# Kernel optimization log

Hardware: AMD Instinct MI355X
Metric: run time of the kernel (lower is better)

Reference implementation:

```python
import jax, jax.numpy as jnp
import numpy as np

B, S, D = 8, 1024, 1024
NEG = -1e9


def setup_inputs() -> dict:
    key = jax.random.key(0)
    ks = jax.random.split(key, 6)
    context = jax.random.normal(ks[0], (B, S, D), dtype=jnp.float32)
    eos_mask = jax.random.randint(ks[1], (B, S, S), 0, 2).astype(jnp.int32)
    scale = 1.0 / np.sqrt(D).astype(np.float32)
    Wq = jax.random.normal(ks[2], (D, D), dtype=jnp.float32) * scale
    bq = jnp.zeros((D,), jnp.float32)
    Wk = jax.random.normal(ks[3], (D, D), dtype=jnp.float32) * scale
    bk = jnp.zeros((D,), jnp.float32)
    ln_a = jnp.ones((D,), jnp.float32)
    ln_b = jnp.zeros((D,), jnp.float32)
    return dict(context=context, eos_mask=eos_mask, Wq=Wq, bq=bq, Wk=Wk, bk=bk,
                ln_a=ln_a, ln_b=ln_b)


def _forward(context, eos_mask, Wq, bq, Wk, bk, ln_a, ln_b):
    d_model = context.shape[-1]
    seq_len = context.shape[1]
    # LayerNorm with torch-style unbiased std (ddof=1)
    mean = context.mean(-1, keepdims=True)
    var = ((context - mean) ** 2).sum(-1, keepdims=True) / (d_model - 1)
    x = ln_a * (context - mean) / (jnp.sqrt(var) + 1e-6) + ln_b

    a = jnp.eye(seq_len, k=1, dtype=jnp.int32)    # super-diagonal
    b = jnp.eye(seq_len, k=0, dtype=jnp.int32)    # diagonal
    c = jnp.eye(seq_len, k=-1, dtype=jnp.int32)   # sub-diagonal
    tri = jnp.triu(jnp.ones((seq_len, seq_len), jnp.float32), 0)

    mask = eos_mask & (a + c)  # [B,S,S] banded + eos mask

    q = x @ Wq.T + bq
    k = x @ Wk.T + bk
    scores = jnp.einsum('bsd,btd->bst', q, k) / d_model
    scores = jnp.where(mask == 0, NEG, scores)
    neibor = jax.nn.softmax(scores, axis=-1)
    neibor = jnp.sqrt(neibor * jnp.swapaxes(neibor, -2, -1) + 1e-9)

    # log-space triangular matmul 'scan'
    t = jnp.where(a == 0, 0.0, jnp.log(neibor + 1e-9)) @ tri  # [B,S,S]
    g = jnp.exp(jnp.einsum('st,btu->bsu', tri, t))
    strict_upper = tri.astype(jnp.int32) - b
    g = jnp.where(strict_upper == 0, 0.0, g)
    g = g + jnp.swapaxes(g, -2, -1) + jnp.where(b == 0, 1e-9, neibor)
    return g, neibor


def reference(context, eos_mask, Wq, bq, Wk, bk, ln_a, ln_b):
    return _forward(context, eos_mask, Wq, bq, Wk, bk, ln_a, ln_b)
```

## Files before the change

kernel.cpp:

```cpp
#include <hip/hip_runtime.h>
#include <math.h>

#define B_ 8
#define S_ 1024
#define D_ 1024
constexpr int BS = B_ * S_;

typedef short bf16x8 __attribute__((ext_vector_type(8)));
typedef float f32x4 __attribute__((ext_vector_type(4)));

__device__ __forceinline__ unsigned short f2bf(float f) {
    unsigned int u = __float_as_uint(f);
    u += 0x7fffu + ((u >> 16) & 1u);
    return (unsigned short)(u >> 16);
}
__device__ __forceinline__ float bf2f(unsigned short h) {
    return __uint_as_float(((unsigned int)h) << 16);
}

__device__ __forceinline__ float block_reduce_sum(float val, float* sh) {
    int tid = threadIdx.x;
    int lane = tid & 63, w = tid >> 6;
    #pragma unroll
    for (int off = 32; off > 0; off >>= 1) val += __shfl_down(val, off, 64);
    if (lane == 0) sh[w] = val;
    __syncthreads();
    int nw = blockDim.x >> 6;
    float total = 0.f;
    for (int i = 0; i < nw; i++) total += sh[i];
    __syncthreads();
    return total;
}

__global__ void ln_kernel(const float* __restrict__ ctx,
                          const float* __restrict__ ln_a,
                          const float* __restrict__ ln_b,
                          unsigned short* __restrict__ xb) {
    __shared__ float sh[4];
    int r = blockIdx.x;
    int tid = threadIdx.x;
    const float* row = ctx + (size_t)r * D_;
    float v[4];
    float s = 0.f;
    #pragma unroll
    for (int i = 0; i < 4; i++) { v[i] = row[tid + i * 256]; s += v[i]; }
    float total = block_reduce_sum(s, sh);
    float mean = total * (1.0f / D_);
    float sq = 0.f;
    #pragma unroll
    for (int i = 0; i < 4; i++) { float d = v[i] - mean; sq += d * d; }
    float varsum = block_reduce_sum(sq, sh);
    float var = varsum * (1.0f / (D_ - 1));
    float inv = 1.0f / (sqrtf(var) + 1e-6f);
    unsigned short* orow = xb + (size_t)r * D_;
    #pragma unroll
    for (int i = 0; i < 4; i++) {
        int d = tid + i * 256;
        orow[d] = f2bf(ln_a[d] * (v[i] - mean) * inv + ln_b[d]);
    }
}

__global__ void transpose2_bf16(const float* __restrict__ inq,
                                const float* __restrict__ ink,
                                unsigned short* __restrict__ outq,
                                unsigned short* __restrict__ outk) {
    __shared__ float t[32][33];
    const float* in = blockIdx.z ? ink : inq;
    unsigned short* out = blockIdx.z ? outk : outq;
    int bx = blockIdx.x * 32, by = blockIdx.y * 32;
    int tx = threadIdx.x, ty = threadIdx.y;
    #pragma unroll
    for (int i = 0; i < 32; i += 8)
        t[ty + i][tx] = in[(size_t)(by + ty + i) * D_ + bx + tx];
    __syncthreads();
    #pragma unroll
    for (int i = 0; i < 32; i += 8)
        out[(size_t)(bx + ty + i) * D_ + by + tx] = f2bf(t[tx][ty + i]);
}

__global__ void bias_terms(const float* __restrict__ Wq, const float* __restrict__ Wk,
                           const float* __restrict__ bq, const float* __restrict__ bk,
                           float* __restrict__ u, float* __restrict__ v,
                           float* __restrict__ c0) {
    int b = blockIdx.x;
    int tid = threadIdx.x;
    float ua[4] = {}, va[4] = {};
    int d0 = b * 128;
    for (int d = d0; d < d0 + 128; d++) {
        float bqd = bq[d], bkd = bk[d];
        const float* wkr = Wk + (size_t)d * D_;
        const float* wqr = Wq + (size_t)d * D_;
        #pragma unroll
        for (int i = 0; i < 4; i++) {
            int c = tid + i * 256;
            ua[i] += wkr[c] * bqd;
            va[i] += wqr[c] * bkd;
        }
    }
    #pragma unroll
    for (int i = 0; i < 4; i++) {
        atomicAdd(&u[tid + i * 256], ua[i]);
        atomicAdd(&v[tid + i * 256], va[i]);
    }
    if (tid < 128) atomicAdd(c0, bq[d0 + tid] * bk[d0 + tid]);
}

__global__ __launch_bounds__(256) void gemm_bt64(
    const unsigned short* __restrict__ A,
    const unsigned short* __restrict__ Bt,
    unsigned short* __restrict__ C,
    int M, int N, int K) {
    __shared__ __align__(16) unsigned short As[64 * 64];
    __shared__ __align__(16) unsigned short Bs[64 * 64];
    const int tid = threadIdx.x;
    const int wave = tid >> 6, lane = tid & 63;
    const int bm = blockIdx.y * 64, bn = blockIdx.x * 64;
    const int lrow8 = lane >> 3;
    const int pchunk = lane & 7;
    const int m_lane = lane & 15, quad = lane >> 4;
    const int wr = wave >> 1, wc = wave & 1;

    f32x4 acc[2][2] = {};

    for (int k0 = 0; k0 < K; k0 += 64) {
        #pragma unroll
        for (int c = 0; c < 2; c++) {
            int row = wave * 16 + c * 8 + lrow8;
            int gchunk = pchunk ^ (row & 7);
            const unsigned short* gpA = A + (size_t)(bm + row) * K + k0 + gchunk * 8;
            const unsigned short* gpB = Bt + (size_t)(bn + row) * K + k0 + gchunk * 8;
            __builtin_amdgcn_global_load_lds(
                (const __attribute__((address_space(1))) void*)gpA,
                (__attribute__((address_space(3))) void*)(As + (wave * 16 + c * 8) * 64),
                16, 0, 0);
            __builtin_amdgcn_global_load_lds(
                (const __attribute__((address_space(1))) void*)gpB,
                (__attribute__((address_space(3))) void*)(Bs + (wave * 16 + c * 8) * 64),
                16, 0, 0);
        }
        __syncthreads();
        #pragma unroll
        for (int kk = 0; kk < 2; kk++) {
            bf16x8 af[2], bfr[2];
            #pragma unroll
            for (int i = 0; i < 2; i++) {
                int row = wr * 32 + i * 16 + m_lane;
                int lchunk = kk * 4 + quad;
                af[i] = *(const bf16x8*)(As + row * 64 + (lchunk ^ (row & 7)) * 8);
            }
            #pragma unroll
            for (int j = 0; j < 2; j++) {
                int row = wc * 32 + j * 16 + m_lane;
                int lchunk = kk * 4 + quad;
                bfr[j] = *(const bf16x8*)(Bs + row * 64 + (lchunk ^ (row & 7)) * 8);
            }
            #pragma unroll
            for (int i = 0; i < 2; i++)
                #pragma unroll
                for (int j = 0; j < 2; j++)
                    acc[i][j] = __builtin_amdgcn_mfma_f32_16x16x32_bf16(
                        af[i], bfr[j], acc[i][j], 0, 0, 0);
        }
        __syncthreads();
    }
    #pragma unroll
    for (int i = 0; i < 2; i++)
        #pragma unroll
        for (int j = 0; j < 2; j++)
            #pragma unroll
            for (int r = 0; r < 4; r++) {
                int row = bm + wr * 32 + i * 16 + quad * 4 + r;
                int col = bn + wc * 32 + j * 16 + m_lane;
                C[(size_t)row * N + col] = f2bf(acc[i][j][r]);
            }
}

__global__ __launch_bounds__(256) void gemm_fused(
    const unsigned short* __restrict__ A,
    const unsigned short* __restrict__ Bt,
    const float* __restrict__ u, const float* __restrict__ v,
    float* __restrict__ ydu, float* __restrict__ ydd,
    float* __restrict__ au, float* __restrict__ av,
    int M, int N, int K) {
    __shared__ __align__(16) unsigned short As[128 * 64];
    __shared__ __align__(16) unsigned short Bs[128 * 64];
    const int tid = threadIdx.x;
    const int wave = tid >> 6, lane = tid & 63;
    const int bm = blockIdx.y * 128, bn = blockIdx.x * 128;
    const int lrow8 = lane >> 3;
    const int pchunk = lane & 7;
    const int m_lane = lane & 15, quad = lane >> 4;
    const int wr = wave >> 1, wc = wave & 1;

    f32x4 acc[4][4] = {};

    for (int k0 = 0; k0 < K; k0 += 64) {
        #pragma unroll
        for (int c = 0; c < 4; c++) {
            int row = wave * 32 + c * 8 + lrow8;
            int gchunk = pchunk ^ (row & 7);
            const unsigned short* gpA = A + (size_t)(bm + row) * K + k0 + gchunk * 8;
            const unsigned short* gpB = Bt + (size_t)(bn + row) * K + k0 + gchunk * 8;
            __builtin_amdgcn_global_load_lds(
                (const __attribute__((address_space(1))) void*)gpA,
                (__attribute__((address_space(3))) void*)(As + (wave * 32 + c * 8) * 64),
                16, 0, 0);
            __builtin_amdgcn_global_load_lds(
                (const __attribute__((address_space(1))) void*)gpB,
                (__attribute__((address_space(3))) void*)(Bs + (wave * 32 + c * 8) * 64),
                16, 0, 0);
        }
        __syncthreads();
        #pragma unroll
        for (int kk = 0; kk < 2; kk++) {
            bf16x8 af[4], bfr[4];
            #pragma unroll
            for (int i = 0; i < 4; i++) {
                int row = wr * 64 + i * 16 + m_lane;
                int lchunk = kk * 4 + quad;
                af[i] = *(const bf16x8*)(As + row * 64 + (lchunk ^ (row & 7)) * 8);
            }
            #pragma unroll
            for (int j = 0; j < 4; j++) {
                int row = wc * 64 + j * 16 + m_lane;
                int lchunk = kk * 4 + quad;
                bfr[j] = *(const bf16x8*)(Bs + row * 64 + (lchunk ^ (row & 7)) * 8);
            }
            #pragma unroll
            for (int i = 0; i < 4; i++)
                #pragma unroll
                for (int j = 0; j < 4; j++)
                    acc[i][j] = __builtin_amdgcn_mfma_f32_16x16x32_bf16(
                        af[i], bfr[j], acc[i][j], 0, 0, 0);
        }
        __syncthreads();
    }

    int cols[4];
    float uvals[4], vvals[4];
    #pragma unroll
    for (int j = 0; j < 4; j++) {
        cols[j] = bn + wc * 64 + j * 16 + m_lane;
        uvals[j] = u[cols[j]];
        vvals[j] = v[cols[j]];
    }
    #pragma unroll
    for (int i = 0; i < 4; i++) {
        #pragma unroll
        for (int r = 0; r < 4; r++) {
            int lrow = wr * 64 + i * 16 + quad * 4 + r;
            int row = bm + lrow;
            int s = row & (S_ - 1);
            bool hu = (s < S_ - 1), hd = (s > 0);
            const unsigned short* xc = A + (size_t)row * D_;
            float pu = 0.f, pd = 0.f, pau = 0.f, pav = 0.f;
            #pragma unroll
            for (int j = 0; j < 4; j++) {
                int c = cols[j];
                float a = acc[i][j][r];
                float xv = bf2f(xc[c]);
                if (hu) pu += a * bf2f(xc[c + D_]);
                if (hd) pd += a * bf2f(xc[c - D_]);
                pau += uvals[j] * xv;
                pav += vvals[j] * xv;
            }
            #pragma unroll
            for (int off = 1; off < 16; off <<= 1) {
                pu += __shfl_xor(pu, off, 64);
                pd += __shfl_xor(pd, off, 64);
                pau += __shfl_xor(pau, off, 64);
                pav += __shfl_xor(pav, off, 64);
            }
            if (m_lane == 0) {
                atomicAdd(&ydu[row], pu);
                atomicAdd(&ydd[row], pd);
                atomicAdd(&au[row], pau);
                atomicAdd(&av[row], pav);
            }
        }
    }
}

__global__ void softmax_prefix(const float* __restrict__ ydu, const float* __restrict__ ydd,
                               const float* __restrict__ au, const float* __restrict__ av,
                               const float* __restrict__ c0p, const int* __restrict__ eos,
                               float* __restrict__ Pup, float* __restrict__ Pdn,
                               float* __restrict__ bg, double* __restrict__ C) {
    __shared__ float pdsh[1024];
    __shared__ double wsum[16];
    int b = blockIdx.x;
    int t = threadIdx.x;
    int r = b * S_ + t;
    float c0 = *c0p;
    const float inv_d = 1.0f / D_;
    bool mu = false, md = false;
    float su = 0.f, sd = 0.f;
    if (t < S_ - 1) {
        mu = eos[(size_t)b * S_ * S_ + (size_t)t * S_ + (t + 1)] != 0;
        su = (ydu[r] + av[r] + au[r + 1] + c0) * inv_d;
    }
    if (t > 0) {
        md = eos[(size_t)b * S_ * S_ + (size_t)t * S_ + (t - 1)] != 0;
        sd = (ydd[r] + av[r] + au[r - 1] + c0) * inv_d;
    }
    float pu, pd, pb;
    if (mu && md) {
        float m = fmaxf(su, sd);
        float eu = expf(su - m), ed = expf(sd - m);
        float inv = 1.0f / (eu + ed);
        pu = eu * inv; pd = ed * inv; pb = 0.f;
    } else if (mu) { pu = 1.f; pd = 0.f; pb = 0.f; }
    else if (md)   { pu = 0.f; pd = 1.f; pb = 0.f; }
    else           { pu = pd = pb = 1.0f / S_; }
    Pup[r] = pu; Pdn[r] = pd; bg[r] = pb;
    pdsh[t] = pd;
    __syncthreads();
    double l = 0.0;
    if (t < S_ - 1) {
        float p = sqrtf(pu * pdsh[t + 1] + 1e-9f) + 1e-9f;
        l = log((double)p);
    }
    int lane = t & 63, w = t >> 6;
    double vv = l;
    #pragma unroll
    for (int off = 1; off < 64; off <<= 1) {
        double o = __shfl_up(vv, off, 64);
        if (lane >= off) vv += o;
    }
    if (lane == 63) wsum[w] = vv;
    __syncthreads();
    if (t == 0) {
        double acc = 0.0;
        #pragma unroll
        for (int i = 0; i < 16; i++) { double x = wsum[i]; wsum[i] = acc; acc += x; }
    }
    __syncthreads();
    vv += wsum[w];
    size_t base = (size_t)b * S_;
    if (t == 0) C[base] = 0.0;
    if (t < S_ - 1) C[base + t + 1] = vv;
}

__global__ void write_out(const float* __restrict__ Pup, const float* __restrict__ Pdn,
                          const float* __restrict__ bg, const double* __restrict__ C,
                          float* __restrict__ out) {
    int r = blockIdx.x;
    int b = r >> 10, s = r & (S_ - 1);
    size_t rowbase = (size_t)r * S_;
    size_t bb = (size_t)b * S_;
    float pu_s = (s < S_ - 1) ? Pup[r] : 0.f;
    float pd_s = (s > 0) ? Pdn[r] : 0.f;
    float bg_s = bg[r];
    double C_s = C[r];
    int t0 = threadIdx.x * 4;
    float* gp = out;
    float* np = out + (size_t)B_ * S_ * S_;
    float4 bgv = *(const float4*)(bg + bb + t0);
    float4 gv, nv;
    #pragma unroll
    for (int j = 0; j < 4; j++) {
        int t = t0 + j;
        float P_st = (t == s + 1) ? pu_s : ((t == s - 1) ? pd_s : bg_s);
        float P_ts;
        if (t == s - 1)      P_ts = Pup[bb + t];
        else if (t == s + 1) P_ts = Pdn[bb + t];
        else                 P_ts = ((const float*)&bgv)[j];
        float neib = sqrtf(P_st * P_ts + 1e-9f);
        float g;
        if (t == s) {
            g = neib;
        } else {
            double diff = (t > s) ? (C[bb + t] - C_s) : (C_s - C[bb + t]);
            g = expf((float)diff) + 1e-9f;
        }
        ((float*)&gv)[j] = g;
        ((float*)&nv)[j] = neib;
    }
    *(float4*)(gp + rowbase + t0) = gv;
    *(float4*)(np + rowbase + t0) = nv;
}

extern "C" void kernel_launch(void* const* d_in, const int* in_sizes, int n_in,
                              void* d_out, int out_size, void* d_ws, size_t ws_size,
                              hipStream_t stream) {
    const float* ctx  = (const float*)d_in[0];
    const int*   eos  = (const int*)d_in[1];
    const float* Wq   = (const float*)d_in[2];
    const float* bq   = (const float*)d_in[3];
    const float* Wk   = (const float*)d_in[4];
    const float* bk   = (const float*)d_in[5];
    const float* ln_a = (const float*)d_in[6];
    const float* ln_b = (const float*)d_in[7];
    float* out = (float*)d_out;

    char* ws = (char*)d_ws;
    size_t off = 0;
    auto alloc = [&](size_t bytes) {
        void* p = ws + off;
        off += (bytes + 255) & ~(size_t)255;
        return p;
    };
    unsigned short* Xb  = (unsigned short*)alloc((size_t)BS * D_ * 2);
    unsigned short* Wqt = (unsigned short*)alloc((size_t)D_ * D_ * 2);
    unsigned short* Wkt = (unsigned short*)alloc((size_t)D_ * D_ * 2);
    unsigned short* Mt  = (unsigned short*)alloc((size_t)D_ * D_ * 2);
    float*  ydu = (float*)alloc(BS * 4);
    float*  ydd = (float*)alloc(BS * 4);
    float*  au  = (float*)alloc(BS * 4);
    float*  av  = (float*)alloc(BS * 4);
    float*  u   = (float*)alloc(D_ * 4);
    float*  v   = (float*)alloc(D_ * 4);
    float*  c0  = (float*)alloc(4);
    size_t zero_bytes = (size_t)((char*)c0 - (char*)ydu) + 256;
    float*  Pup = (float*)alloc(BS * 4);
    float*  Pdn = (float*)alloc(BS * 4);
    float*  bg  = (float*)alloc(BS * 4);
    double* Cp  = (double*)alloc(BS * 8);

    hipMemsetAsync(ydu, 0, zero_bytes, stream);
    ln_kernel<<<BS, 256, 0, stream>>>(ctx, ln_a, ln_b, Xb);
    transpose2_bf16<<<dim3(32, 32, 2), dim3(32, 8), 0, stream>>>(Wq, Wk, Wqt, Wkt);
    bias_terms<<<8, 256, 0, stream>>>(Wq, Wk, bq, bk, u, v, c0);
    gemm_bt64<<<dim3(16, 16), 256, 0, stream>>>(Wkt, Wqt, Mt, D_, D_, D_);
    gemm_fused<<<dim3(8, 64), 256, 0, stream>>>(Xb, Mt, u, v, ydu, ydd, au, av,
                                                BS, D_, D_);
    softmax_prefix<<<B_, 1024, 0, stream>>>(ydu, ydd, au, av, c0, eos, Pup, Pdn, bg, Cp);
    write_out<<<BS, 256, 0, stream>>>(Pup, Pdn, bg, Cp, out);
}
```

Measured before the change: 217.8 us.

## Move bias dot products into LayerNorm and merge weight prep kernels

The per-row dot products of the normalized input with the bias-derived vectors u and v are now computed inside the LayerNorm kernel, which receives them after a new combined prep kernel. This removes two extra shuffle reductions, four atomics per row and the extra x loads from the GEMM epilogue. The weight transpose and bias-term kernels are merged into one launch, and LayerNorm now uses vectorized float4 loads and ushort4 stores. The cost is two more block reductions in LayerNorm and a serialized dependency of LayerNorm on the prep kernel.

```diff
diff --git a/kernel.cpp b/kernel.cpp
--- a/kernel.cpp
+++ b/kernel.cpp
@@ -35,74 +35,86 @@
 __global__ void ln_kernel(const float* __restrict__ ctx,
                           const float* __restrict__ ln_a,
                           const float* __restrict__ ln_b,
-                          unsigned short* __restrict__ xb) {
+                          const float* __restrict__ u,
+                          const float* __restrict__ v,
+                          unsigned short* __restrict__ xb,
+                          float* __restrict__ au, float* __restrict__ av) {
     __shared__ float sh[4];
     int r = blockIdx.x;
     int tid = threadIdx.x;
+    int d0 = tid * 4;
     const float* row = ctx + (size_t)r * D_;
-    float v[4];
-    float s = 0.f;
-    #pragma unroll
-    for (int i = 0; i < 4; i++) { v[i] = row[tid + i * 256]; s += v[i]; }
+    float4 x4 = *(const float4*)(row + d0);
+    float s = x4.x + x4.y + x4.z + x4.w;
     float total = block_reduce_sum(s, sh);
     float mean = total * (1.0f / D_);
-    float sq = 0.f;
-    #pragma unroll
-    for (int i = 0; i < 4; i++) { float d = v[i] - mean; sq += d * d; }
+    float dx = x4.x - mean, dy = x4.y - mean, dz = x4.z - mean, dw = x4.w - mean;
+    float sq = dx * dx + dy * dy + dz * dz + dw * dw;
     float varsum = block_reduce_sum(sq, sh);
     float var = varsum * (1.0f / (D_ - 1));
     float inv = 1.0f / (sqrtf(var) + 1e-6f);
-    unsigned short* orow = xb + (size_t)r * D_;
-    #pragma unroll
-    for (int i = 0; i < 4; i++) {
-        int d = tid + i * 256;
-        orow[d] = f2bf(ln_a[d] * (v[i] - mean) * inv + ln_b[d]);
-    }
-}
-
-__global__ void transpose2_bf16(const float* __restrict__ inq,
-                                const float* __restrict__ ink,
-                                unsigned short* __restrict__ outq,
-                                unsigned short* __restrict__ outk) {
-    __shared__ float t[32][33];
-    const float* in = blockIdx.z ? ink : inq;
-    unsigned short* out = blockIdx.z ? outk : outq;
-    int bx = blockIdx.x * 32, by = blockIdx.y * 32;
-    int tx = threadIdx.x, ty = threadIdx.y;
-    #pragma unroll
-    for (int i = 0; i < 32; i += 8)
-        t[ty + i][tx] = in[(size_t)(by + ty + i) * D_ + bx + tx];
-    __syncthreads();
-    #pragma unroll
-    for (int i = 0; i < 32; i += 8)
-        out[(size_t)(bx + ty + i) * D_ + by + tx] = f2bf(t[tx][ty + i]);
-}
-
-__global__ void bias_terms(const float* __restrict__ Wq, const float* __restrict__ Wk,
-                           const float* __restrict__ bq, const float* __restrict__ bk,
-                           float* __restrict__ u, float* __restrict__ v,
-                           float* __restrict__ c0) {
-    int b = blockIdx.x;
+    float4 a4 = *(const float4*)(ln_a + d0);
+    float4 b4 = *(const float4*)(ln_b + d0);
+    float y0 = a4.x * dx * inv + b4.x;
+    float y1 = a4.y * dy * inv + b4.y;
+    float y2 = a4.z * dz * inv + b4.z;
+    float y3 = a4.w * dw * inv + b4.w;
+    ushort4 o;
+    o.x = f2bf(y0); o.y = f2bf(y1); o.z = f2bf(y2); o.w = f2bf(y3);
+    *(ushort4*)(xb + (size_t)r * D_ + d0) = o;
+    float4 u4 = *(const float4*)(u + d0);
+    float4 v4 = *(const float4*)(v + d0);
+    float pu = u4.x * y0 + u4.y * y1 + u4.z * y2 + u4.w * y3;
+    float pv = v4.x * y0 + v4.y * y1 + v4.z * y2 + v4.w * y3;
+    pu = block_reduce_sum(pu, sh);
+    pv = block_reduce_sum(pv, sh);
+    if (tid == 0) { au[r] = pu; av[r] = pv; }
+}
+
+__global__ void prep_kernel(const float* __restrict__ Wq, const float* __restrict__ Wk,
+                            const float* __restrict__ bq, const float* __restrict__ bk,
+                            unsigned short* __restrict__ Wqt,
+                            unsigned short* __restrict__ Wkt,
+                            float* __restrict__ u, float* __restrict__ v,
+                            float* __restrict__ c0) {
+    int bid = blockIdx.x;
     int tid = threadIdx.x;
-    float ua[4] = {}, va[4] = {};
-    int d0 = b * 128;
-    for (int d = d0; d < d0 + 128; d++) {
-        float bqd = bq[d], bkd = bk[d];
-        const float* wkr = Wk + (size_t)d * D_;
-        const float* wqr = Wq + (size_t)d * D_;
+    if (bid < 2048) {
+        __shared__ float t[32][33];
+        const float* in = (bid < 1024) ? Wq : Wk;
+        unsigned short* out = (bid < 1024) ? Wqt : Wkt;
+        int bb = bid & 1023;
+        int bx = (bb & 31) * 32, by = (bb >> 5) * 32;
+        int tx = tid & 31, ty = tid >> 5;
+        #pragma unroll
+        for (int i = 0; i < 32; i += 8)
+            t[ty + i][tx] = in[(size_t)(by + ty + i) * D_ + bx + tx];
+        __syncthreads();
+        #pragma unroll
+        for (int i = 0; i < 32; i += 8)
+            out[(size_t)(bx + ty + i) * D_ + by + tx] = f2bf(t[tx][ty + i]);
+    } else {
+        int b = bid - 2048;
+        float ua[4] = {}, va[4] = {};
+        int d0 = b * 128;
+        for (int d = d0; d < d0 + 128; d++) {
+            float bqd = bq[d], bkd = bk[d];
+            const float* wkr = Wk + (size_t)d * D_;
+            const float* wqr = Wq + (size_t)d * D_;
+            #pragma unroll
+            for (int i = 0; i < 4; i++) {
+                int c = tid + i * 256;
+                ua[i] += wkr[c] * bqd;
+                va[i] += wqr[c] * bkd;
+            }
+        }
         #pragma unroll
         for (int i = 0; i < 4; i++) {
-            int c = tid + i * 256;
-            ua[i] += wkr[c] * bqd;
-            va[i] += wqr[c] * bkd;
-        }
-    }
-    #pragma unroll
-    for (int i = 0; i < 4; i++) {
-        atomicAdd(&u[tid + i * 256], ua[i]);
-        atomicAdd(&v[tid + i * 256], va[i]);
-    }
-    if (tid < 128) atomicAdd(c0, bq[d0 + tid] * bk[d0 + tid]);
+            atomicAdd(&u[tid + i * 256], ua[i]);
+            atomicAdd(&v[tid + i * 256], va[i]);
+        }
+        if (tid < 128) atomicAdd(c0, bq[d0 + tid] * bk[d0 + tid]);
+    }
 }
 
 __global__ __launch_bounds__(256) void gemm_bt64(
@@ -178,9 +190,7 @@
 __global__ __launch_bounds__(256) void gemm_fused(
     const unsigned short* __restrict__ A,
     const unsigned short* __restrict__ Bt,
-    const float* __restrict__ u, const float* __restrict__ v,
     float* __restrict__ ydu, float* __restrict__ ydd,
-    float* __restrict__ au, float* __restrict__ av,
     int M, int N, int K) {
     __shared__ __align__(16) unsigned short As[128 * 64];
     __shared__ __align__(16) unsigned short Bs[128 * 64];
@@ -237,13 +247,8 @@
     }
 
     int cols[4];
-    float uvals[4], vvals[4];
-    #pragma unroll
-    for (int j = 0; j < 4; j++) {
-        cols[j] = bn + wc * 64 + j * 16 + m_lane;
-        uvals[j] = u[cols[j]];
-        vvals[j] = v[cols[j]];
-    }
+    #pragma unroll
+    for (int j = 0; j < 4; j++) cols[j] = bn + wc * 64 + j * 16 + m_lane;
     #pragma unroll
     for (int i = 0; i < 4; i++) {
         #pragma unroll
@@ -253,29 +258,22 @@
             int s = row & (S_ - 1);
             bool hu = (s < S_ - 1), hd = (s > 0);
             const unsigned short* xc = A + (size_t)row * D_;
-            float pu = 0.f, pd = 0.f, pau = 0.f, pav = 0.f;
+            float pu = 0.f, pd = 0.f;
             #pragma unroll
             for (int j = 0; j < 4; j++) {
                 int c = cols[j];
                 float a = acc[i][j][r];
-                float xv = bf2f(xc[c]);
                 if (hu) pu += a * bf2f(xc[c + D_]);
                 if (hd) pd += a * bf2f(xc[c - D_]);
-                pau += uvals[j] * xv;
-                pav += vvals[j] * xv;
             }
             #pragma unroll
             for (int off = 1; off < 16; off <<= 1) {
                 pu += __shfl_xor(pu, off, 64);
                 pd += __shfl_xor(pd, off, 64);
-                pau += __shfl_xor(pau, off, 64);
-                pav += __shfl_xor(pav, off, 64);
             }
             if (m_lane == 0) {
                 atomicAdd(&ydu[row], pu);
                 atomicAdd(&ydd[row], pd);
-                atomicAdd(&au[row], pau);
-                atomicAdd(&av[row], pav);
             }
         }
     }
@@ -406,24 +404,22 @@
     unsigned short* Mt  = (unsigned short*)alloc((size_t)D_ * D_ * 2);
     float*  ydu = (float*)alloc(BS * 4);
     float*  ydd = (float*)alloc(BS * 4);
-    float*  au  = (float*)alloc(BS * 4);
-    float*  av  = (float*)alloc(BS * 4);
     float*  u   = (float*)alloc(D_ * 4);
     float*  v   = (float*)alloc(D_ * 4);
     float*  c0  = (float*)alloc(4);
     size_t zero_bytes = (size_t)((char*)c0 - (char*)ydu) + 256;
+    float*  au  = (float*)alloc(BS * 4);
+    float*  av  = (float*)alloc(BS * 4);
     float*  Pup = (float*)alloc(BS * 4);
     float*  Pdn = (float*)alloc(BS * 4);
     float*  bg  = (float*)alloc(BS * 4);
     double* Cp  = (double*)alloc(BS * 8);
 
     hipMemsetAsync(ydu, 0, zero_bytes, stream);
-    ln_kernel<<<BS, 256, 0, stream>>>(ctx, ln_a, ln_b, Xb);
-    transpose2_bf16<<<dim3(32, 32, 2), dim3(32, 8), 0, stream>>>(Wq, Wk, Wqt, Wkt);
-    bias_terms<<<8, 256, 0, stream>>>(Wq, Wk, bq, bk, u, v, c0);
+    prep_kernel<<<2056, 256, 0, stream>>>(Wq, Wk, bq, bk, Wqt, Wkt, u, v, c0);
+    ln_kernel<<<BS, 256, 0, stream>>>(ctx, ln_a, ln_b, u, v, Xb, au, av);
     gemm_bt64<<<dim3(16, 16), 256, 0, stream>>>(Wkt, Wqt, Mt, D_, D_, D_);
-    gemm_fused<<<dim3(8, 64), 256, 0, stream>>>(Xb, Mt, u, v, ydu, ydd, au, av,
-                                                BS, D_, D_);
+    gemm_fused<<<dim3(8, 64), 256, 0, stream>>>(Xb, Mt, ydu, ydd, BS, D_, D_);
     softmax_prefix<<<B_, 1024, 0, stream>>>(ydu, ydd, au, av, c0, eos, Pup, Pdn, bg, Cp);
     write_out<<<BS, 256, 0, stream>>>(Pup, Pdn, bg, Cp, out);
 }
```

Measured after the change: 220.0 us. About the same (+1.0%).
